# Optimization experiments

Measured on AMD Instinct MI355X. Metric: run time of the kernel, lower is better.

## Reference

```python
import jax, jax.numpy as jnp
import numpy as np

V, T, NS, NH, E, H = 4, 4, 100000, 12288, 100000, 64
NEG_SLOPE = 0.01  # nn.LeakyReLU default


def setup_inputs() -> dict:
    key = jax.random.key(0)
    k1, k2, k3, k4, k5 = jax.random.split(key, 5)
    x = jax.random.normal(k1, (V, T, NS), dtype=jnp.float32)          # per-var, per-t scalar node features
    src_idx = jax.random.randint(k2, (V, T, E), 0, NS, dtype=jnp.int32)
    dst_idx = jax.random.randint(k3, (V, T, E), 0, NH, dtype=jnp.int32)
    W = jax.random.normal(k4, (V, T, H), dtype=jnp.float32)            # GraphConv weight, in_feats=1 -> [1,H] per etype
    b = jax.random.normal(k5, (V, T, H), dtype=jnp.float32) * 0.02     # GraphConv bias per etype
    return {"x": x, "W": W, "b": b, "src_idx": src_idx, "dst_idx": dst_idx, "n_healpix": NH}


def reference(x, W, b, src_idx, dst_idx, n_healpix):
    # x: [V,T,NS]; W,b: [V,T,H]; src_idx,dst_idx: [V,T,E]
    x = jnp.nan_to_num(x, nan=0.0)

    def conv_scalar(x_v, src, dst):
        # x_v: [T,NS] (all timestep features for this var), src/dst: [E] for ONE edge type
        ones = jnp.ones(src.shape, x_v.dtype)
        deg_out = jax.ops.segment_sum(ones, src, num_segments=NS)       # out-degree of src nodes
        deg_in = jax.ops.segment_sum(ones, dst, num_segments=n_healpix)  # in-degree of dst nodes
        norm_src = jax.lax.rsqrt(jnp.maximum(deg_out, 1.0))
        norm_dst = jax.lax.rsqrt(jnp.maximum(deg_in, 1.0))
        msg = x_v[:, src] * norm_src[src]                                # [T,E] gather
        agg = jax.vmap(lambda m: jax.ops.segment_sum(m, dst, num_segments=n_healpix))(msg)  # [T,NH]
        return agg * norm_dst                                            # norm='both'

    # HeteroGraphConv bug-faithful: for each var, EVERY per-t' conv is applied to each x[:,t]
    # s[v, t', t, n] = normalized scatter of x[v,t] through edges of etype t'
    s = jax.vmap(lambda xv, sv, dv: jax.vmap(lambda se, de: conv_scalar(xv, se, de))(sv, dv))(
        x, src_idx, dst_idx)                                             # [V,T',T,NH]

    # in_feats=1: linear is outer product with W row; bias + LeakyReLU inside each conv, sum over etypes t'
    h = jax.nn.leaky_relu(s[..., None] * W[:, :, None, None, :] + b[:, :, None, None, :],
                          negative_slope=NEG_SLOPE)                      # [V,T',T,NH,H]
    out = h.sum(axis=1)                                                  # aggregate='sum' over edge types -> [V,T,NH,H]
    # final stacking: stack over t (dim=1) then over vars (dim=1) -> [NH, V, T, H]
    return jnp.transpose(out, (2, 0, 1, 3))
```

## Files before the change

### kernel.cpp

```cpp
#include <hip/hip_runtime.h>
#include <math.h>

#define V    4
#define T    4
#define NSRC 100000
#define NHX  12288
#define E    100000
#define H    64
#define VT   16

#define SL    8
#define SLE   (E/SL)
#define RCH   2
#define RBINS (NSRC/RCH)
#define RW    (RBINS/4)
#define HF    8
#define HE    (E/HF)
#define NW    (NSRC/4)
#define NCH   12
#define NPB   8

#define S1_TRANS  391
#define S1_CNT    (RCH*HF*VT)
#define S1_DHIST  (SL*VT)
#define S2_SCAN   (NCH*VT)
#define S2_NSFIN  391

__global__ void __launch_bounds__(1024)
s1_kernel(const float* __restrict__ x, const int* __restrict__ src,
          const int* __restrict__ dst, float4* __restrict__ x4,
          unsigned int* __restrict__ cnt_part, unsigned int* __restrict__ ph,
          unsigned int* __restrict__ blocksum) {
    __shared__ unsigned int lds[RW];
    const int b = blockIdx.x, tid = threadIdx.x;

    if (b < S1_TRANS) {
        const int g = b * 1024 + tid;
        if (g < V * NSRC) {
            const int v = g / NSRC, s = g - v * NSRC;
            const float* xr = x + (size_t)v * T * NSRC + s;
            float a0 = xr[0], a1 = xr[NSRC], a2 = xr[2 * NSRC], a3 = xr[3 * NSRC];
            float4 r;
            r.x = (a0 == a0) ? a0 : 0.0f;
            r.y = (a1 == a1) ? a1 : 0.0f;
            r.z = (a2 == a2) ? a2 : 0.0f;
            r.w = (a3 == a3) ? a3 : 0.0f;
            x4[g] = r;
        }
        return;
    }
    if (b < S1_TRANS + S1_CNT) {
        const int idx = b - S1_TRANS;
        const int rg = idx & 1;
        const int hf = (idx >> 1) & 7;
        const int vt = idx >> 4;
        const int lo = rg * RBINS;
        for (int i = tid; i < RW; i += 1024) lds[i] = 0u;
        __syncthreads();
        const int* s_row = src + vt * E + hf * HE;
        for (int e = tid; e < HE; e += 1024) {
            const unsigned r = (unsigned)(s_row[e] - lo);
            if (r < RBINS) atomicAdd(&lds[r >> 2], 1u << ((r & 3) * 8));
        }
        __syncthreads();
        unsigned int* outp = cnt_part + ((size_t)hf * VT + vt) * NW + rg * RW;
        for (int i = tid; i < RW; i += 1024) outp[i] = lds[i];
        return;
    }
    {
        const int idx = b - (S1_TRANS + S1_CNT);
        const int sl = idx & 7, vt = idx >> 3;
        for (int i = tid; i < NHX; i += 1024) lds[i] = 0u;
        __syncthreads();
        const int* d_row = dst + vt * E + sl * SLE;
        for (int e = tid; e < SLE; e += 1024)
            atomicAdd(&lds[d_row[e]], 1u);
        __syncthreads();
        unsigned int* outp = ph + ((size_t)vt * SL + sl) * NHX;
        for (int i = tid; i < NHX; i += 1024) outp[i] = lds[i];
        const int lane = tid & 63, wv = tid >> 6;
        if (wv < NCH) {
            unsigned int s = 0;
#pragma unroll
            for (int i = 0; i < 16; ++i) s += lds[wv * 1024 + i * 64 + lane];
#pragma unroll
            for (int off = 32; off > 0; off >>= 1)
                s += (unsigned int)__shfl_down((int)s, off, 64);
            if (lane == 0) atomicAdd(&blocksum[vt * NCH + wv], s);
        }
    }
}

__global__ void __launch_bounds__(1024)
s2_kernel(const unsigned int* __restrict__ cnt_part,
          const unsigned int* __restrict__ ph,
          const unsigned int* __restrict__ blocksum,
          float4* __restrict__ ns4,
          unsigned int* __restrict__ start,
          unsigned int* __restrict__ colstart,
          unsigned int* __restrict__ degs) {
    const int b = blockIdx.x, tid = threadIdx.x;

    if (b < S2_SCAN) {
        const int vt = b & 15, ch = b >> 4;
        const int lane = tid & 63, wv = tid >> 6;
        const int d = ch * 1024 + tid;
        __shared__ unsigned int wsum[16];
        __shared__ unsigned int sbase;
        if (tid == 0) {
            unsigned int base = 0;
            for (int c = 0; c < ch; ++c) base += blocksum[vt * NCH + c];
            sbase = base;
        }
        unsigned int h[SL];
        unsigned int tot = 0;
#pragma unroll
        for (int s = 0; s < SL; ++s) {
            h[s] = ph[((size_t)vt * SL + s) * NHX + d];
            tot += h[s];
        }
        unsigned int incl = tot;
#pragma unroll
        for (int off = 1; off < 64; off <<= 1) {
            const unsigned int vup = (unsigned int)__shfl_up((int)incl, off, 64);
            if (lane >= off) incl += vup;
        }
        if (lane == 63) wsum[wv] = incl;
        __syncthreads();
        if (tid == 0) {
            unsigned int run = sbase;
#pragma unroll
            for (int w = 0; w < 16; ++w) { const unsigned int t2 = wsum[w]; wsum[w] = run; run += t2; }
        }
        __syncthreads();
        const unsigned int excl = wsum[wv] + (incl - tot);
        const size_t vd = (size_t)vt * NHX + d;
        colstart[vd] = excl;
        degs[vd]     = tot;
        unsigned int acc = excl;
#pragma unroll
        for (int s = 0; s < SL; ++s) {
            start[((size_t)vt * SL + s) * NHX + d] = acc;
            acc += h[s];
        }
        return;
    }
    {
        const int g = (b - S2_SCAN) * 1024 + tid;
        if (g >= VT * NW) return;
        const int vt = g / NW;
        unsigned c0 = 0, c1 = 0, c2 = 0, c3 = 0;
#pragma unroll
        for (int hf = 0; hf < HF; ++hf) {
            const unsigned w = cnt_part[(size_t)hf * VT * NW + g
                                        - (size_t)vt * NW + (size_t)vt * NW];
            c0 += w & 0xFFu; c1 += (w >> 8) & 0xFFu;
            c2 += (w >> 16) & 0xFFu; c3 += w >> 24;
        }
        float4 r;
        r.x = rsqrtf(fmaxf((float)c0, 1.0f));
        r.y = rsqrtf(fmaxf((float)c1, 1.0f));
        r.z = rsqrtf(fmaxf((float)c2, 1.0f));
        r.w = rsqrtf(fmaxf((float)c3, 1.0f));
        ns4[g] = r;
    }
}

__global__ void __launch_bounds__(1024)
s3_reorder(const int* __restrict__ src, const int* __restrict__ dst,
           const unsigned int* __restrict__ start, int* __restrict__ sorted) {
    const int b = blockIdx.x;
    const int k = b & 7, j = b >> 3;
    const int vt = 2 * k + (j & 1);
    const int sl = j >> 1;
    __shared__ unsigned int pos[NHX];
    const unsigned int* st = start + ((size_t)vt * SL + sl) * NHX;
    for (int i = threadIdx.x; i < NHX; i += 1024) pos[i] = st[i];
    __syncthreads();
    const int* s_row = src + vt * E + sl * SLE;
    const int* d_row = dst + vt * E + sl * SLE;
    int* outp = sorted + (size_t)vt * E;
    for (int e = threadIdx.x; e < SLE; e += 1024) {
        const int d = d_row[e];
        const int s = s_row[e];
        const unsigned int p = atomicAdd(&pos[d], 1u);
        outp[p] = s;
    }
}

__global__ void __launch_bounds__(256)
s4_accum(const float4* __restrict__ x4, const int* __restrict__ sorted,
         const float* __restrict__ ns,
         const unsigned int* __restrict__ colstart,
         const unsigned int* __restrict__ degs,
         float4* __restrict__ sval) {
    const int b = blockIdx.x;
    const int k = b & 7, j = b >> 3;
    const int vt = 2 * k + (j & 1);
    const int chunk = j >> 1;
    const int d = chunk * 256 + threadIdx.x;
    const int v = vt >> 2;
    const size_t vd = (size_t)vt * NHX + d;
    const unsigned int base = colstart[vd];
    const unsigned int deg  = degs[vd];
    const float nd = rsqrtf(fmaxf((float)deg, 1.0f));
    const int*    srt    = sorted + (size_t)vt * E;
    const float*  ns_row = ns + (size_t)vt * NSRC;
    const float4* x_row  = x4 + (size_t)v * NSRC;
    float4 acc = make_float4(0.f, 0.f, 0.f, 0.f);
    unsigned int i = 0;
    for (; i + 2 <= deg; i += 2) {
        const int s0 = srt[base + i];
        const int s1 = srt[base + i + 1];
        const float4 xa = x_row[s0]; const float na = ns_row[s0];
        const float4 xb = x_row[s1]; const float nb = ns_row[s1];
        acc.x += xa.x * na + xb.x * nb;
        acc.y += xa.y * na + xb.y * nb;
        acc.z += xa.z * na + xb.z * nb;
        acc.w += xa.w * na + xb.w * nb;
    }
    if (i < deg) {
        const int s0 = srt[base + i];
        const float4 xa = x_row[s0]; const float na = ns_row[s0];
        acc.x += xa.x * na; acc.y += xa.y * na;
        acc.z += xa.z * na; acc.w += xa.w * na;
    }
    acc.x *= nd; acc.y *= nd; acc.z *= nd; acc.w *= nd;
    sval[vd] = acc;
}

__global__ void __launch_bounds__(256)
s5_epilogue(const float4* __restrict__ sval, const float* __restrict__ Wm,
            const float* __restrict__ bm, float* __restrict__ out) {
    const int n0  = blockIdx.x * NPB;
    const int tid = threadIdx.x;
    __shared__ float sW[VT * H];
    __shared__ float sb[VT * H];
    __shared__ float sv[VT][T][NPB];

    for (int i = tid; i < VT * H; i += 256) { sW[i] = Wm[i]; sb[i] = bm[i]; }
    if (tid < VT * NPB) {
        const int vt = tid >> 3, n = tid & 7;
        const float4 r = sval[(size_t)vt * NHX + n0 + n];
        sv[vt][0][n] = r.x; sv[vt][1][n] = r.y;
        sv[vt][2][n] = r.z; sv[vt][3][n] = r.w;
    }
    __syncthreads();

    const int v  = tid >> 6;
    const int t  = (tid >> 4) & 3;
    const int hb = (tid & 15) * 4;
    float4 Wr[4], Br[4];
#pragma unroll
    for (int tp = 0; tp < 4; ++tp) {
        const int wi = (v * 4 + tp) * H + hb;
        Wr[tp] = *(const float4*)&sW[wi];
        Br[tp] = *(const float4*)&sb[wi];
    }
#pragma unroll
    for (int n = 0; n < NPB; ++n) {
        float4 o = make_float4(0.f, 0.f, 0.f, 0.f);
#pragma unroll
        for (int tp = 0; tp < 4; ++tp) {
            const float s = sv[v * 4 + tp][t][n];
            float a;
            a = fmaf(s, Wr[tp].x, Br[tp].x); o.x += (a > 0.f) ? a : 0.01f * a;
            a = fmaf(s, Wr[tp].y, Br[tp].y); o.y += (a > 0.f) ? a : 0.01f * a;
            a = fmaf(s, Wr[tp].z, Br[tp].z); o.z += (a > 0.f) ? a : 0.01f * a;
            a = fmaf(s, Wr[tp].w, Br[tp].w); o.w += (a > 0.f) ? a : 0.01f * a;
        }
        ((float4*)(out + (size_t)(n0 + n) * (V * T * H)))[tid] = o;
    }
}

extern "C" void kernel_launch(void* const* d_in, const int* in_sizes, int n_in,
                              void* d_out, int out_size, void* d_ws, size_t ws_size,
                              hipStream_t stream) {
    const float* x   = (const float*)d_in[0];
    const float* Wm  = (const float*)d_in[1];
    const float* bm  = (const float*)d_in[2];
    const int*   src = (const int*)d_in[3];
    const int*   dst = (const int*)d_in[4];
    float* out = (float*)d_out;

    char* ws = (char*)d_ws;
    size_t off = 0;
    float4* x4 = (float4*)(ws + off);                   off += (size_t)V * NSRC * 16;
    float4* sval = (float4*)(ws + off);                 off += (size_t)VT * NHX * 16;
    float4* ns4 = (float4*)(ws + off);                  off += (size_t)VT * NSRC * 4;
    unsigned int* ph = (unsigned int*)(ws + off);       off += (size_t)VT * SL * NHX * 4;
    unsigned int* start = (unsigned int*)(ws + off);    off += (size_t)VT * SL * NHX * 4;
    unsigned int* colstart = (unsigned int*)(ws + off); off += (size_t)VT * NHX * 4;
    unsigned int* degs = (unsigned int*)(ws + off);     off += (size_t)VT * NHX * 4;
    unsigned int* blocksum = (unsigned int*)(ws + off); off += 1024;
    unsigned int* cnt_part = (unsigned int*)(ws + off); off += (size_t)HF * VT * NW * 4;
    int* sorted = (int*)(ws + off);                     off += (size_t)VT * E * 4;
    float* ns = (float*)ns4;

    hipMemsetAsync(blocksum, 0, VT * NCH * sizeof(unsigned int), stream);
    s1_kernel<<<S1_TRANS + S1_CNT + S1_DHIST, 1024, 0, stream>>>(
        x, src, dst, x4, cnt_part, ph, blocksum);
    s2_kernel<<<S2_SCAN + S2_NSFIN, 1024, 0, stream>>>(
        cnt_part, ph, blocksum, ns4, start, colstart, degs);
    s3_reorder<<<SL * VT, 1024, 0, stream>>>(src, dst, start, sorted);
    s4_accum<<<768, 256, 0, stream>>>(x4, sorted, ns, colstart, degs, sval);
    s5_epilogue<<<NHX / NPB, 256, 0, stream>>>(sval, Wm, bm, out);
}
```

Before: 148.7 us.

## Split gather across lanes, double dst-histogram slices, drop memset, use nontemporal stores

Doubles the number of dst slices in the histogram and reorder stages for more parallelism. Replaces the atomic blocksum accumulation, which needed a memset, with per-slice chunk sums that are reduced by a wave in the scan. Splits each destination row's gather across two lanes combined with a shuffle, and launches twice as many accumulate blocks to expose more memory-level parallelism. Writes the large output with nontemporal stores to avoid cache pollution. The risk is more per-slice arrays and scan work, plus lower per-lane ILP in the gather.

```diff
diff --git a/kernel.cpp b/kernel.cpp
--- a/kernel.cpp
+++ b/kernel.cpp
@@ -9,7 +9,7 @@
 #define H    64
 #define VT   16
 
-#define SL    8
+#define SL    16
 #define SLE   (E/SL)
 #define RCH   2
 #define RBINS (NSRC/RCH)
@@ -26,11 +26,13 @@
 #define S2_SCAN   (NCH*VT)
 #define S2_NSFIN  391
 
+typedef float vf4 __attribute__((ext_vector_type(4)));
+
 __global__ void __launch_bounds__(1024)
 s1_kernel(const float* __restrict__ x, const int* __restrict__ src,
           const int* __restrict__ dst, float4* __restrict__ x4,
           unsigned int* __restrict__ cnt_part, unsigned int* __restrict__ ph,
-          unsigned int* __restrict__ blocksum) {
+          unsigned int* __restrict__ cs) {
     __shared__ unsigned int lds[RW];
     const int b = blockIdx.x, tid = threadIdx.x;
 
@@ -69,7 +71,7 @@
     }
     {
         const int idx = b - (S1_TRANS + S1_CNT);
-        const int sl = idx & 7, vt = idx >> 3;
+        const int sl = idx & 15, vt = idx >> 4;
         for (int i = tid; i < NHX; i += 1024) lds[i] = 0u;
         __syncthreads();
         const int* d_row = dst + vt * E + sl * SLE;
@@ -86,7 +88,7 @@
 #pragma unroll
             for (int off = 32; off > 0; off >>= 1)
                 s += (unsigned int)__shfl_down((int)s, off, 64);
-            if (lane == 0) atomicAdd(&blocksum[vt * NCH + wv], s);
+            if (lane == 0) cs[((size_t)vt * SL + sl) * NCH + wv] = s;
         }
     }
 }
@@ -94,7 +96,7 @@
 __global__ void __launch_bounds__(1024)
 s2_kernel(const unsigned int* __restrict__ cnt_part,
           const unsigned int* __restrict__ ph,
-          const unsigned int* __restrict__ blocksum,
+          const unsigned int* __restrict__ cs,
           float4* __restrict__ ns4,
           unsigned int* __restrict__ start,
           unsigned int* __restrict__ colstart,
@@ -107,10 +109,15 @@
         const int d = ch * 1024 + tid;
         __shared__ unsigned int wsum[16];
         __shared__ unsigned int sbase;
-        if (tid == 0) {
-            unsigned int base = 0;
-            for (int c = 0; c < ch; ++c) base += blocksum[vt * NCH + c];
-            sbase = base;
+        if (wv == 0) {
+            unsigned int p = 0;
+            if (lane < SL)
+                for (int c = 0; c < ch; ++c)
+                    p += cs[((size_t)vt * SL + lane) * NCH + c];
+#pragma unroll
+            for (int off = 8; off > 0; off >>= 1)
+                p += (unsigned int)__shfl_down((int)p, off, 64);
+            if (lane == 0) sbase = p;
         }
         unsigned int h[SL];
         unsigned int tot = 0;
@@ -148,12 +155,10 @@
     {
         const int g = (b - S2_SCAN) * 1024 + tid;
         if (g >= VT * NW) return;
-        const int vt = g / NW;
         unsigned c0 = 0, c1 = 0, c2 = 0, c3 = 0;
 #pragma unroll
         for (int hf = 0; hf < HF; ++hf) {
-            const unsigned w = cnt_part[(size_t)hf * VT * NW + g
-                                        - (size_t)vt * NW + (size_t)vt * NW];
+            const unsigned w = cnt_part[(size_t)hf * VT * NW + g];
             c0 += w & 0xFFu; c1 += (w >> 8) & 0xFFu;
             c2 += (w >> 16) & 0xFFu; c3 += w >> 24;
         }
@@ -198,35 +203,32 @@
     const int k = b & 7, j = b >> 3;
     const int vt = 2 * k + (j & 1);
     const int chunk = j >> 1;
-    const int d = chunk * 256 + threadIdx.x;
+    const int d = chunk * 128 + (threadIdx.x >> 1);
+    const int half = threadIdx.x & 1;
     const int v = vt >> 2;
     const size_t vd = (size_t)vt * NHX + d;
     const unsigned int base = colstart[vd];
     const unsigned int deg  = degs[vd];
-    const float nd = rsqrtf(fmaxf((float)deg, 1.0f));
     const int*    srt    = sorted + (size_t)vt * E;
     const float*  ns_row = ns + (size_t)vt * NSRC;
     const float4* x_row  = x4 + (size_t)v * NSRC;
     float4 acc = make_float4(0.f, 0.f, 0.f, 0.f);
-    unsigned int i = 0;
-    for (; i + 2 <= deg; i += 2) {
-        const int s0 = srt[base + i];
-        const int s1 = srt[base + i + 1];
-        const float4 xa = x_row[s0]; const float na = ns_row[s0];
-        const float4 xb = x_row[s1]; const float nb = ns_row[s1];
-        acc.x += xa.x * na + xb.x * nb;
-        acc.y += xa.y * na + xb.y * nb;
-        acc.z += xa.z * na + xb.z * nb;
-        acc.w += xa.w * na + xb.w * nb;
-    }
-    if (i < deg) {
-        const int s0 = srt[base + i];
-        const float4 xa = x_row[s0]; const float na = ns_row[s0];
+    for (unsigned int i = half; i < deg; i += 2) {
+        const int s = srt[base + i];
+        const float4 xa = x_row[s];
+        const float  na = ns_row[s];
         acc.x += xa.x * na; acc.y += xa.y * na;
         acc.z += xa.z * na; acc.w += xa.w * na;
     }
-    acc.x *= nd; acc.y *= nd; acc.z *= nd; acc.w *= nd;
-    sval[vd] = acc;
+    acc.x += __shfl_xor(acc.x, 1, 64);
+    acc.y += __shfl_xor(acc.y, 1, 64);
+    acc.z += __shfl_xor(acc.z, 1, 64);
+    acc.w += __shfl_xor(acc.w, 1, 64);
+    if (half == 0) {
+        const float nd = rsqrtf(fmaxf((float)deg, 1.0f));
+        acc.x *= nd; acc.y *= nd; acc.z *= nd; acc.w *= nd;
+        sval[vd] = acc;
+    }
 }
 
 __global__ void __launch_bounds__(256)
@@ -269,7 +271,8 @@
             a = fmaf(s, Wr[tp].z, Br[tp].z); o.z += (a > 0.f) ? a : 0.01f * a;
             a = fmaf(s, Wr[tp].w, Br[tp].w); o.w += (a > 0.f) ? a : 0.01f * a;
         }
-        ((float4*)(out + (size_t)(n0 + n) * (V * T * H)))[tid] = o;
+        vf4* dstp = (vf4*)(out + (size_t)(n0 + n) * (V * T * H)) + tid;
+        __builtin_nontemporal_store(*(vf4*)&o, dstp);
     }
 }
 
@@ -292,17 +295,16 @@
     unsigned int* start = (unsigned int*)(ws + off);    off += (size_t)VT * SL * NHX * 4;
     unsigned int* colstart = (unsigned int*)(ws + off); off += (size_t)VT * NHX * 4;
     unsigned int* degs = (unsigned int*)(ws + off);     off += (size_t)VT * NHX * 4;
-    unsigned int* blocksum = (unsigned int*)(ws + off); off += 1024;
+    unsigned int* cs = (unsigned int*)(ws + off);       off += (size_t)VT * SL * NCH * 4;
     unsigned int* cnt_part = (unsigned int*)(ws + off); off += (size_t)HF * VT * NW * 4;
     int* sorted = (int*)(ws + off);                     off += (size_t)VT * E * 4;
     float* ns = (float*)ns4;
 
-    hipMemsetAsync(blocksum, 0, VT * NCH * sizeof(unsigned int), stream);
     s1_kernel<<<S1_TRANS + S1_CNT + S1_DHIST, 1024, 0, stream>>>(
-        x, src, dst, x4, cnt_part, ph, blocksum);
+        x, src, dst, x4, cnt_part, ph, cs);
     s2_kernel<<<S2_SCAN + S2_NSFIN, 1024, 0, stream>>>(
-        cnt_part, ph, blocksum, ns4, start, colstart, degs);
+        cnt_part, ph, cs, ns4, start, colstart, degs);
     s3_reorder<<<SL * VT, 1024, 0, stream>>>(src, dst, start, sorted);
-    s4_accum<<<768, 256, 0, stream>>>(x4, sorted, ns, colstart, degs, sval);
+    s4_accum<<<1536, 256, 0, stream>>>(x4, sorted, ns, colstart, degs, sval);
     s5_epilogue<<<NHX / NPB, 256, 0, stream>>>(sval, Wm, bm, out);
 }
```

Result: faster. 145.3 us (-2.3%).
